# Performance work log

Measured on AMD Instinct MI355X. Metric: run time of the kernel, lower is better.

## Reference

```python
import jax, jax.numpy as jnp
import numpy as np

B, T, I, H = 1024, 64, 64, 1024
FUTURE = 16


def lstm_cell(x_t, h, c, Wih, Whh, b_ih, b_hh):
    # torch LSTMCell gate order: i, f, g, o; weights are (4H, in)
    gates = x_t @ Wih.T + h @ Whh.T + b_ih + b_hh  # (B, 4H)
    i, f, g, o = jnp.split(gates, 4, axis=-1)
    i = jax.nn.sigmoid(i)
    f = jax.nn.sigmoid(f)
    g = jnp.tanh(g)
    o = jax.nn.sigmoid(o)
    c_new = f * c + i * g
    h_new = o * jnp.tanh(c_new)
    return h_new, c_new


def setup_inputs() -> dict:
    key = jax.random.key(0)
    ks = jax.random.split(key, 12)
    s1 = 1.0 / np.sqrt(H)
    inp = {
        "x": jax.random.normal(ks[0], (B, T, I), dtype=jnp.float32),
        "W_ih1": jax.random.uniform(ks[1], (4 * H, I), jnp.float32, -s1, s1),
        "W_hh1": jax.random.uniform(ks[2], (4 * H, H), jnp.float32, -s1, s1),
        "b_ih1": jax.random.uniform(ks[3], (4 * H,), jnp.float32, -s1, s1),
        "b_hh1": jax.random.uniform(ks[4], (4 * H,), jnp.float32, -s1, s1),
        "W_ih2": jax.random.uniform(ks[5], (4 * H, H), jnp.float32, -s1, s1),
        "W_hh2": jax.random.uniform(ks[6], (4 * H, H), jnp.float32, -s1, s1),
        "b_ih2": jax.random.uniform(ks[7], (4 * H,), jnp.float32, -s1, s1),
        "b_hh2": jax.random.uniform(ks[8], (4 * H,), jnp.float32, -s1, s1),
        "W_lin": jax.random.uniform(ks[9], (I, H), jnp.float32, -s1, s1),
        "b_lin": jax.random.uniform(ks[10], (I,), jnp.float32, -s1, s1),
        "future": FUTURE,
    }
    return inp


def reference(x, W_ih1, W_hh1, b_ih1, b_hh1, W_ih2, W_hh2, b_ih2, b_hh2,
              W_lin, b_lin, future):
    b_size = x.shape[0]
    zeros = jnp.zeros((b_size, H), dtype=x.dtype)

    def two_layer_step(h1, c1, h2, c2, x_t):
        h1, c1 = lstm_cell(x_t, h1, c1, W_ih1, W_hh1, b_ih1, b_hh1)
        h2, c2 = lstm_cell(h1, h2, c2, W_ih2, W_hh2, b_ih2, b_hh2)
        out = h2 @ W_lin.T + b_lin  # (B, I)
        return h1, c1, h2, c2, out

    def step(carry, x_t):
        h1, c1, h2, c2 = carry
        h1, c1, h2, c2, out = two_layer_step(h1, c1, h2, c2, x_t)
        return (h1, c1, h2, c2), out

    xs = jnp.transpose(x, (1, 0, 2))  # (T, B, I)
    carry, outs = jax.lax.scan(step, (zeros, zeros, zeros, zeros), xs)

    if future > 0:
        def fstep(carry, _):
            h1, c1, h2, c2, out = carry
            h1, c1, h2, c2, out = two_layer_step(h1, c1, h2, c2, out)
            return (h1, c1, h2, c2, out), out

        h1, c1, h2, c2 = carry
        _, fouts = jax.lax.scan(fstep, (h1, c1, h2, c2, outs[-1]),
                                None, length=future)
        outs = jnp.concatenate([outs, fouts], axis=0)

    return jnp.transpose(outs, (1, 0, 2))  # (B, T+future, I)
```

## Files before the change

### kernel.cpp

```cpp
#include <hip/hip_runtime.h>


#define B_   1024
#define T_   64
#define I_   64
#define H_   1024
#define FUT_ 16
#define NST_ (T_ + FUT_)
#define SROW 2176

typedef _Float16 half8_t  __attribute__((ext_vector_type(8)));
typedef float    float4_t __attribute__((ext_vector_type(4)));

typedef __attribute__((address_space(1))) const unsigned int g_u32;
typedef __attribute__((address_space(3))) unsigned int l_u32;

__device__ __forceinline__ void load_lds16(const _Float16* g, _Float16* l) {
    __builtin_amdgcn_global_load_lds((g_u32*)g, (l_u32*)l, 16, 0, 0);
}

__device__ __forceinline__ float sigmoid_f(float x) {
    x = fminf(fmaxf(x, -30.f), 30.f);
    return __fdividef(1.f, 1.f + __expf(-x));
}
__device__ __forceinline__ float tanh_f(float x) {
    x = fminf(fmaxf(x, -15.f), 15.f);
    float e = __expf(2.f * x);
    return 1.f - 2.f * __fdividef(1.f, e + 1.f);
}

__global__ void convert_all(const float* __restrict__ x,
    const float* __restrict__ Wih1, const float* __restrict__ Whh1,
    const float* __restrict__ bih1, const float* __restrict__ bhh1,
    const float* __restrict__ Wih2, const float* __restrict__ Whh2,
    const float* __restrict__ bih2, const float* __restrict__ bhh2,
    const float* __restrict__ Wlin,
    _Float16* __restrict__ W1p, _Float16* __restrict__ W2p,
    _Float16* __restrict__ Wlp,
    _Float16* __restrict__ S0x, _Float16* __restrict__ S1x,
    float* __restrict__ b1, float* __restrict__ b2)
{
    size_t idx = (size_t)blockIdx.x * 256 + threadIdx.x;
    const size_t nc1 = 589824;
    const size_t nc2 = 1048576;
    const size_t nc3 = 8192;
    const size_t nx  = 65536;
    if (idx < nc1) {
        int c = (int)idx;
        int lane = c & 63, g = (c >> 6) & 3, rem = c >> 8;
        int j = rem % 36, hgrp = rem / 36;
        int row = (g << 10) + hgrp * 16 + (lane & 15);
        int kb = j * 32 + (lane >> 4) * 8;
        _Float16* o = &W1p[(size_t)c * 8];
        if (kb < 1024) {
            #pragma unroll
            for (int i = 0; i < 8; ++i) o[i] = (_Float16)Whh1[(size_t)row * 1024 + kb + i];
        } else if (kb < 1088) {
            #pragma unroll
            for (int i = 0; i < 8; ++i) o[i] = (_Float16)Wih1[row * 64 + (kb - 1024) + i];
        } else {
            #pragma unroll
            for (int i = 0; i < 8; ++i) o[i] = (_Float16)0.f;
        }
    } else if ((idx -= nc1) < nc2) {
        int c = (int)idx;
        int lane = c & 63, g = (c >> 6) & 3, rem = c >> 8;
        int j = rem & 63, hgrp = rem >> 6;
        int row = (g << 10) + hgrp * 16 + (lane & 15);
        int kb = j * 32 + (lane >> 4) * 8;
        _Float16* o = &W2p[(size_t)c * 8];
        if (kb < 1024) {
            #pragma unroll
            for (int i = 0; i < 8; ++i) o[i] = (_Float16)Wih2[(size_t)row * 1024 + kb + i];
        } else {
            #pragma unroll
            for (int i = 0; i < 8; ++i) o[i] = (_Float16)Whh2[(size_t)row * 1024 + kb - 1024 + i];
        }
    } else if ((idx -= nc2) < nc3) {
        int c = (int)idx;
        int lane = c & 63, j = (c >> 6) & 31, hgrp = c >> 11;
        int row = hgrp * 16 + (lane & 15);
        int kb = j * 32 + (lane >> 4) * 8;
        _Float16* o = &Wlp[(size_t)c * 8];
        #pragma unroll
        for (int i = 0; i < 8; ++i) o[i] = (_Float16)Wlin[(size_t)row * 1024 + kb + i];
    } else if ((idx -= nc3) < nx) {
        int b = (int)(idx >> 6), i = (int)(idx & 63);
        S0x[(size_t)b * SROW + i] = (_Float16)x[(size_t)b * (T_ * I_) + i];
    } else if ((idx -= nx) < nx) {
        int b = (int)(idx >> 6), i = (int)(idx & 63);
        S1x[(size_t)b * SROW + i] = (_Float16)x[(size_t)b * (T_ * I_) + 64 + i];
    } else if ((idx -= nx) < 4096) {
        b1[idx] = bih1[idx] + bhh1[idx];
    } else if ((idx -= 4096) < 4096) {
        b2[idx] = bih2[idx] + bhh2[idx];
    }
}

__device__ __forceinline__ void gemm_body(_Float16* sA,
    const _Float16* __restrict__ Alo, const _Float16* __restrict__ Ahi,
    const _Float16* __restrict__ Wp, const int iters, const int Ksh,
    const float* __restrict__ bias, float* __restrict__ cvec,
    _Float16* __restrict__ hdst, const int unit)
{
    const int tid = threadIdx.x;
    const int lane = tid & 63, w = tid >> 6;
    const int hw = w & 1, kh = w >> 1;
    const int lr = lane & 15, lq = lane >> 4;
    const int ht = ((unit & 7) << 2) | ((unit >> 3) & 3);
    const int mt = unit >> 5;
    const int h0 = ht * 32, m0 = mt * 64;
    const int hgrp = ht * 2 + hw;

    const char* wptr = (const char*)Wp
        + ((size_t)hgrp * (2 * Ksh) + (size_t)kh * Ksh) * 4096
        + (size_t)lane * 16;

    const int srow0 = tid >> 4, pg = tid & 15;
    const int gg = pg ^ (srow0 & 15);
    const _Float16* asrc = (gg < 8 ? Alo : Ahi) + (gg & 7) * 8
                         + (size_t)(m0 + srow0) * SROW;
    _Float16* ldst = sA + tid * 8;

    const int ag0 = ((kh * 8 + lq) ^ lr) * 8;
    const int ag1 = ((kh * 8 + 4 + lq) ^ lr) * 8;

    float4_t acc[4][4];
    #pragma unroll
    for (int g = 0; g < 4; ++g)
        #pragma unroll
        for (int rt = 0; rt < 4; ++rt)
            #pragma unroll
            for (int e = 0; e < 4; ++e) acc[g][rt][e] = 0.f;

    half8_t bfc[8], bfn[8];
    #pragma unroll
    for (int q = 0; q < 8; ++q)
        bfc[q] = *(const half8_t*)(wptr + q * 1024);

    for (int i = 0; i < iters; ++i) {
        #pragma unroll
        for (int s = 0; s < 4; ++s)
            load_lds16(asrc + (size_t)(srow0 + s * 16 - srow0) * 0
                       + (size_t)s * 16 * SROW + (size_t)i * 64,
                       ldst + s * 2048);
        __syncthreads();

        if (i + 1 < iters) {
            const char* wn = wptr + 8192;
            #pragma unroll
            for (int q = 0; q < 8; ++q)
                bfn[q] = *(const half8_t*)(wn + q * 1024);
        }
        #pragma unroll
        for (int ks = 0; ks < 2; ++ks) {
            const int ag = ks ? ag1 : ag0;
            half8_t af[4];
            #pragma unroll
            for (int rt = 0; rt < 4; ++rt)
                af[rt] = *(const half8_t*)&sA[(rt * 16 + lr) * 128 + ag];
            #pragma unroll
            for (int g = 0; g < 4; ++g)
                #pragma unroll
                for (int rt = 0; rt < 4; ++rt)
                    acc[g][rt] = __builtin_amdgcn_mfma_f32_16x16x32_f16(
                        af[rt], bfc[ks * 4 + g], acc[g][rt], 0, 0, 0);
        }
        __syncthreads();
        wptr += 8192;
        #pragma unroll
        for (int q = 0; q < 8; ++q) bfc[q] = bfn[q];
    }

    float* scr = (float*)sA;
    #pragma unroll
    for (int gp = 0; gp < 2; ++gp) {
        if (kh == 1) {
            #pragma unroll
            for (int g2 = 0; g2 < 2; ++g2)
                #pragma unroll
                for (int rt = 0; rt < 4; ++rt) {
                    int slot = ((hw * 2 + g2) * 4 + rt) * 64 + lane;
                    *(float4_t*)&scr[slot * 4] = acc[gp * 2 + g2][rt];
                }
        }
        __syncthreads();
        if (kh == 0) {
            #pragma unroll
            for (int g2 = 0; g2 < 2; ++g2)
                #pragma unroll
                for (int rt = 0; rt < 4; ++rt) {
                    int slot = ((hw * 2 + g2) * 4 + rt) * 64 + lane;
                    acc[gp * 2 + g2][rt] += *(const float4_t*)&scr[slot * 4];
                }
        }
        __syncthreads();
    }
    if (kh != 0) return;

    const int j = h0 + hw * 16 + lr;
    const float bi = bias[j], bff = bias[1024 + j];
    const float bg = bias[2048 + j], bo = bias[3072 + j];
    #pragma unroll
    for (int rt = 0; rt < 4; ++rt) {
        #pragma unroll
        for (int e = 0; e < 4; ++e) {
            const int brow = m0 + rt * 16 + lq * 4 + e;
            float gi = sigmoid_f(acc[0][rt][e] + bi);
            float gf = sigmoid_f(acc[1][rt][e] + bff);
            float gv = tanh_f(acc[2][rt][e] + bg);
            float go = sigmoid_f(acc[3][rt][e] + bo);
            const size_t ci = (size_t)brow * 1024 + j;
            float cn = gf * cvec[ci] + gi * gv;
            cvec[ci] = cn;
            hdst[(size_t)brow * SROW + j] = (_Float16)(go * tanh_f(cn));
        }
    }
}

__device__ __forceinline__ void proj_body(_Float16* sA,
    const _Float16* __restrict__ A, const _Float16* __restrict__ Wp,
    const float* __restrict__ blin, float* __restrict__ outp,
    _Float16* __restrict__ xdst, const int unit)
{
    const int iters = 8;
    const int tid = threadIdx.x;
    const int lane = tid & 63, w = tid >> 6;
    const int hw = w & 1, kh = w >> 1;
    const int lr = lane & 15, lq = lane >> 4;
    const int ht = unit & 1, mt = unit >> 1;
    const int h0 = ht * 32, m0 = mt * 64;
    const int hgrp = ht * 2 + hw;

    const char* wptr = (const char*)Wp
        + ((size_t)hgrp * 32 + (size_t)kh * 16) * 1024 + (size_t)lane * 16;

    const int srow0 = tid >> 4, pg = tid & 15;
    const int gg = pg ^ (srow0 & 15);
    const _Float16* asrc = A + (size_t)(gg >> 3) * 512 + (gg & 7) * 8
                         + (size_t)(m0 + srow0) * SROW;
    _Float16* ldst = sA + tid * 8;
    const int ag0 = ((kh * 8 + lq) ^ lr) * 8;
    const int ag1 = ((kh * 8 + 4 + lq) ^ lr) * 8;

    float4_t acc[4];
    #pragma unroll
    for (int rt = 0; rt < 4; ++rt)
        #pragma unroll
        for (int e = 0; e < 4; ++e) acc[rt][e] = 0.f;

    half8_t b0 = *(const half8_t*)(wptr);
    half8_t b1v = *(const half8_t*)(wptr + 1024);
    for (int i = 0; i < iters; ++i) {
        #pragma unroll
        for (int s = 0; s < 4; ++s)
            load_lds16(asrc + (size_t)s * 16 * SROW + (size_t)i * 64,
                       ldst + s * 2048);
        __syncthreads();
        half8_t n0, n1;
        if (i + 1 < iters) {
            n0 = *(const half8_t*)(wptr + 2048);
            n1 = *(const half8_t*)(wptr + 3072);
        }
        half8_t af;
        #pragma unroll
        for (int rt = 0; rt < 4; ++rt) {
            af = *(const half8_t*)&sA[(rt * 16 + lr) * 128 + ag0];
            acc[rt] = __builtin_amdgcn_mfma_f32_16x16x32_f16(af, b0, acc[rt], 0, 0, 0);
        }
        #pragma unroll
        for (int rt = 0; rt < 4; ++rt) {
            af = *(const half8_t*)&sA[(rt * 16 + lr) * 128 + ag1];
            acc[rt] = __builtin_amdgcn_mfma_f32_16x16x32_f16(af, b1v, acc[rt], 0, 0, 0);
        }
        __syncthreads();
        wptr += 2048;
        b0 = n0; b1v = n1;
    }

    float* scr = (float*)sA;
    if (kh == 1) {
        #pragma unroll
        for (int rt = 0; rt < 4; ++rt) {
            int slot = (hw * 4 + rt) * 64 + lane;
            *(float4_t*)&scr[slot * 4] = acc[rt];
        }
    }
    __syncthreads();
    if (kh != 0) return;
    #pragma unroll
    for (int rt = 0; rt < 4; ++rt) {
        int slot = (hw * 4 + rt) * 64 + lane;
        acc[rt] += *(const float4_t*)&scr[slot * 4];
    }

    const int j = h0 + hw * 16 + lr;
    const float bj = blin[j];
    #pragma unroll
    for (int rt = 0; rt < 4; ++rt) {
        #pragma unroll
        for (int e = 0; e < 4; ++e) {
            const int brow = m0 + rt * 16 + lq * 4 + e;
            float s = acc[rt][e] + bj;
            outp[(size_t)brow * (NST_ * I_) + j] = s;
            if (xdst) xdst[(size_t)brow * SROW + j] = (_Float16)s;
        }
    }
}

struct StepArgs {
    int nL2, nL1, nProj, nCopy;
    const _Float16 *l2Alo, *l2Ahi; _Float16* l2H; float* c2;
    const _Float16 *l1Alo, *l1Ahi; _Float16* l1H; float* c1;
    const _Float16* pA; float* pOut; _Float16* pXdst;
    const float* xsrc; _Float16* xdst;
    const _Float16 *W1p, *W2p, *Wlp;
    const float *b1, *b2, *blin;
};

__global__ __launch_bounds__(256, 3) void fused_step(StepArgs a) {
    __shared__ __align__(16) _Float16 sA[8192];
    int bid = blockIdx.x;
    if (bid < a.nL2) {
        gemm_body(sA, a.l2Alo, a.l2Ahi, a.W2p, 16, 32, a.b2, a.c2, a.l2H, bid);
    } else if ((bid -= a.nL2) < a.nL1) {
        gemm_body(sA, a.l1Alo, a.l1Ahi, a.W1p, 9, 18, a.b1, a.c1, a.l1H, bid);
    } else if ((bid -= a.nL1) < a.nProj) {
        proj_body(sA, a.pA, a.Wlp, a.blin, a.pOut, a.pXdst, bid);
    } else {
        bid -= a.nProj;
        int base = bid * 256 + threadIdx.x;
        for (int k = base; k < B_ * I_; k += a.nCopy * 256) {
            int b = k >> 6, i = k & 63;
            a.xdst[(size_t)b * SROW + i] = (_Float16)a.xsrc[(size_t)b * (T_ * I_) + i];
        }
    }
}

extern "C" void kernel_launch(void* const* d_in, const int* in_sizes, int n_in,
                              void* d_out, int out_size, void* d_ws, size_t ws_size,
                              hipStream_t stream) {
    (void)in_sizes; (void)n_in; (void)out_size; (void)ws_size;
    const float* x    = (const float*)d_in[0];
    const float* Wih1 = (const float*)d_in[1];
    const float* Whh1 = (const float*)d_in[2];
    const float* bih1 = (const float*)d_in[3];
    const float* bhh1 = (const float*)d_in[4];
    const float* Wih2 = (const float*)d_in[5];
    const float* Whh2 = (const float*)d_in[6];
    const float* bih2 = (const float*)d_in[7];
    const float* bhh2 = (const float*)d_in[8];
    const float* Wlin = (const float*)d_in[9];
    const float* blin = (const float*)d_in[10];
    float* out = (float*)d_out;

    char* p = (char*)d_ws;
    auto alloc = [&](size_t bytes) {
        char* r = p; p += (bytes + 255) & ~(size_t)255; return r;
    };
    _Float16* W1p = (_Float16*)alloc((size_t)4096 * 1152 * 2);
    _Float16* W2p = (_Float16*)alloc((size_t)4096 * 2048 * 2);
    _Float16* Wlp = (_Float16*)alloc((size_t)64 * 1024 * 2);
    _Float16* S[3];
    for (int i = 0; i < 3; ++i) S[i] = (_Float16*)alloc((size_t)B_ * SROW * 2);
    float* c1 = (float*)alloc((size_t)B_ * H_ * 4);
    float* c2 = (float*)alloc((size_t)B_ * H_ * 4);
    float* b1 = (float*)alloc(4096 * 4);
    float* b2 = (float*)alloc(4096 * 4);

    for (int i = 0; i < 3; ++i)
        hipMemsetAsync(S[i], 0, (size_t)B_ * SROW * 2, stream);
    hipMemsetAsync(c1, 0, (size_t)B_ * H_ * 4, stream);
    hipMemsetAsync(c2, 0, (size_t)B_ * H_ * 4, stream);

    {
        const size_t total = 589824 + 1048576 + 8192 + 65536 + 65536 + 8192;
        convert_all<<<(int)((total + 255) / 256), 256, 0, stream>>>(
            x, Wih1, Whh1, bih1, bhh1, Wih2, Whh2, bih2, bhh2, Wlin,
            W1p, W2p, Wlp, S[0] + 1024, S[1] + 1024, b1, b2);
    }

    StepArgs a{};
    a.W1p = W1p; a.W2p = W2p; a.Wlp = Wlp;
    a.b1 = b1; a.b2 = b2; a.blin = blin;
    a.c1 = c1; a.c2 = c2;

    {
        StepArgs q = a;
        q.nL2 = 0; q.nL1 = 512; q.nProj = 0; q.nCopy = 0;
        q.l1Alo = S[0]; q.l1Ahi = S[0] + 576; q.l1H = S[1];
        fused_step<<<512, 256, 0, stream>>>(q);
    }

    for (int t = 0; t <= 62; ++t) {
        _Float16* Sp = S[t % 3];
        _Float16* Sq = S[(t + 1) % 3];
        _Float16* Sn = S[(t + 2) % 3];
        StepArgs q = a;
        q.nL2 = 512; q.nL1 = 512;
        q.nProj = (t >= 1) ? 32 : 0;
        q.nCopy = (t <= 61) ? 16 : 0;
        q.l2Alo = Sq; q.l2Ahi = Sp + 1152; q.l2H = Sq + 1152;
        q.l1Alo = Sq; q.l1Ahi = Sq + 576; q.l1H = Sn;
        q.pA = Sp + 1152; q.pOut = out + (size_t)(t - 1) * I_; q.pXdst = nullptr;
        q.xsrc = x + (size_t)(t + 2) * I_; q.xdst = Sn + 1024;
        int grid = q.nL2 + q.nL1 + q.nProj + q.nCopy;
        fused_step<<<grid, 256, 0, stream>>>(q);
    }

    {
        StepArgs q = a;
        q.nL2 = 512; q.nL1 = 0; q.nProj = 32; q.nCopy = 0;
        q.l2Alo = S[1]; q.l2Ahi = S[0] + 1152; q.l2H = S[1] + 1152;
        q.pA = S[0] + 1152; q.pOut = out + (size_t)62 * I_; q.pXdst = nullptr;
        fused_step<<<544, 256, 0, stream>>>(q);
    }
    {
        StepArgs q = a;
        q.nL2 = 0; q.nL1 = 0; q.nProj = 32; q.nCopy = 0;
        q.pA = S[1] + 1152; q.pOut = out + (size_t)63 * I_; q.pXdst = S[1] + 1024;
        fused_step<<<32, 256, 0, stream>>>(q);
    }

    for (int t = T_; t < NST_; ++t) {
        _Float16* Sp = S[t % 3];
        _Float16* Sq = S[(t + 1) % 3];
        {
            StepArgs q = a;
            q.nL2 = 0; q.nL1 = 512; q.nProj = 0; q.nCopy = 0;
            q.l1Alo = Sp; q.l1Ahi = Sp + 576; q.l1H = Sq;
            fused_step<<<512, 256, 0, stream>>>(q);
        }
        {
            StepArgs q = a;
            q.nL2 = 512; q.nL1 = 0; q.nProj = 0; q.nCopy = 0;
            q.l2Alo = Sq; q.l2Ahi = Sp + 1152; q.l2H = Sq + 1152;
            fused_step<<<512, 256, 0, stream>>>(q);
        }
        {
            StepArgs q = a;
            q.nL2 = 0; q.nL1 = 0; q.nProj = 32; q.nCopy = 0;
            q.pA = Sq + 1152; q.pOut = out + (size_t)t * I_;
            q.pXdst = (t + 1 < NST_) ? (Sq + 1024) : nullptr;
            fused_step<<<32, 256, 0, stream>>>(q);
        }
    }
}
```

Before: 3.686 ms.

## Fold output projection into layer-1 weights for future steps and double-buffer LDS

For the autoregressive future steps, the layer-1 input weights are precomposed with the linear projection (W_ih1·W_lin, with bias folded in), so layer 1 reads h2 directly instead of waiting for a separate projection kernel. Each future step drops from three launches to two, and the projection output now runs alongside the layer-1 GEMM. Separately, the GEMM A-tile staging is double-buffered in LDS, removing one barrier per k-iteration, which doubles shared memory per block. The composed weights are rounded to fp16 after the product, which changes rounding relative to the reference path.

Result: faster. 3.561 ms (-3.4%).

```diff
diff --git a/kernel.cpp b/kernel.cpp
--- a/kernel.cpp
+++ b/kernel.cpp
@@ -97,7 +97,44 @@
     }
 }
 
-__device__ __forceinline__ void gemm_body(_Float16* sA,
+__global__ void compose_pack(const float* __restrict__ Wih1,
+    const float* __restrict__ Whh1, const float* __restrict__ Wlin,
+    const float* __restrict__ blin, const float* __restrict__ b1in,
+    _Float16* __restrict__ W1c2, float* __restrict__ bc1)
+{
+    size_t idx = (size_t)blockIdx.x * 256 + threadIdx.x;
+    const size_t NC = 1048576;
+    if (idx < NC) {
+        int c = (int)idx;
+        int lane = c & 63, g = (c >> 6) & 3, rem = c >> 8;
+        int j = rem & 63, hgrp = rem >> 6;
+        int row = (g << 10) + hgrp * 16 + (lane & 15);
+        int kb = j * 32 + (lane >> 4) * 8;
+        _Float16* o = &W1c2[(size_t)c * 8];
+        if (kb < 1024) {
+            #pragma unroll
+            for (int i = 0; i < 8; ++i) o[i] = (_Float16)Whh1[(size_t)row * 1024 + kb + i];
+        } else {
+            const int h = kb - 1024;
+            float acc[8] = {0, 0, 0, 0, 0, 0, 0, 0};
+            for (int i2 = 0; i2 < 64; ++i2) {
+                float wv = Wih1[row * 64 + i2];
+                const float* wl = &Wlin[(size_t)i2 * 1024 + h];
+                #pragma unroll
+                for (int e = 0; e < 8; ++e) acc[e] += wv * wl[e];
+            }
+            #pragma unroll
+            for (int e = 0; e < 8; ++e) o[e] = (_Float16)acc[e];
+        }
+    } else if ((idx -= NC) < 4096) {
+        int n = (int)idx;
+        float s = b1in[n];
+        for (int i2 = 0; i2 < 64; ++i2) s += Wih1[n * 64 + i2] * blin[i2];
+        bc1[n] = s;
+    }
+}
+
+__device__ __forceinline__ void gemm_body(_Float16* sAb,
     const _Float16* __restrict__ Alo, const _Float16* __restrict__ Ahi,
     const _Float16* __restrict__ Wp, const int iters, const int Ksh,
     const float* __restrict__ bias, float* __restrict__ cvec,
@@ -120,7 +157,6 @@
     const int gg = pg ^ (srow0 & 15);
     const _Float16* asrc = (gg < 8 ? Alo : Ahi) + (gg & 7) * 8
                          + (size_t)(m0 + srow0) * SROW;
-    _Float16* ldst = sA + tid * 8;
 
     const int ag0 = ((kh * 8 + lq) ^ lr) * 8;
     const int ag1 = ((kh * 8 + 4 + lq) ^ lr) * 8;
@@ -138,15 +174,19 @@
     for (int q = 0; q < 8; ++q)
         bfc[q] = *(const half8_t*)(wptr + q * 1024);
 
+    #pragma unroll
+    for (int s = 0; s < 4; ++s)
+        load_lds16(asrc + (size_t)s * 16 * SROW, sAb + tid * 8 + s * 2048);
+
     for (int i = 0; i < iters; ++i) {
-        #pragma unroll
-        for (int s = 0; s < 4; ++s)
-            load_lds16(asrc + (size_t)(srow0 + s * 16 - srow0) * 0
-                       + (size_t)s * 16 * SROW + (size_t)i * 64,
-                       ldst + s * 2048);
         __syncthreads();
-
+        _Float16* cur = sAb + (i & 1) * 8192;
         if (i + 1 < iters) {
+            _Float16* nxt = sAb + ((i + 1) & 1) * 8192;
+            const _Float16* an = asrc + (size_t)(i + 1) * 64;
+            #pragma unroll
+            for (int s = 0; s < 4; ++s)
+                load_lds16(an + (size_t)s * 16 * SROW, nxt + tid * 8 + s * 2048);
             const char* wn = wptr + 8192;
             #pragma unroll
             for (int q = 0; q < 8; ++q)
@@ -155,24 +195,22 @@
         #pragma unroll
         for (int ks = 0; ks < 2; ++ks) {
             const int ag = ks ? ag1 : ag0;
-            half8_t af[4];
-            #pragma unroll
-            for (int rt = 0; rt < 4; ++rt)
-                af[rt] = *(const half8_t*)&sA[(rt * 16 + lr) * 128 + ag];
-            #pragma unroll
-            for (int g = 0; g < 4; ++g)
+            #pragma unroll
+            for (int rt = 0; rt < 4; ++rt) {
+                half8_t af = *(const half8_t*)&cur[(rt * 16 + lr) * 128 + ag];
                 #pragma unroll
-                for (int rt = 0; rt < 4; ++rt)
+                for (int g = 0; g < 4; ++g)
                     acc[g][rt] = __builtin_amdgcn_mfma_f32_16x16x32_f16(
-                        af[rt], bfc[ks * 4 + g], acc[g][rt], 0, 0, 0);
-        }
-        __syncthreads();
+                        af, bfc[ks * 4 + g], acc[g][rt], 0, 0, 0);
+            }
+        }
         wptr += 8192;
         #pragma unroll
         for (int q = 0; q < 8; ++q) bfc[q] = bfn[q];
     }
-
-    float* scr = (float*)sA;
+    __syncthreads();
+
+    float* scr = (float*)sAb;
     #pragma unroll
     for (int gp = 0; gp < 2; ++gp) {
         if (kh == 1) {
@@ -221,7 +259,7 @@
 __device__ __forceinline__ void proj_body(_Float16* sA,
     const _Float16* __restrict__ A, const _Float16* __restrict__ Wp,
     const float* __restrict__ blin, float* __restrict__ outp,
-    _Float16* __restrict__ xdst, const int unit)
+    const int unit)
 {
     const int iters = 8;
     const int tid = threadIdx.x;
@@ -301,32 +339,32 @@
         #pragma unroll
         for (int e = 0; e < 4; ++e) {
             const int brow = m0 + rt * 16 + lq * 4 + e;
-            float s = acc[rt][e] + bj;
-            outp[(size_t)brow * (NST_ * I_) + j] = s;
-            if (xdst) xdst[(size_t)brow * SROW + j] = (_Float16)s;
+            outp[(size_t)brow * (NST_ * I_) + j] = acc[rt][e] + bj;
         }
     }
 }
 
 struct StepArgs {
     int nL2, nL1, nProj, nCopy;
-    const _Float16 *l2Alo, *l2Ahi; _Float16* l2H; float* c2;
-    const _Float16 *l1Alo, *l1Ahi; _Float16* l1H; float* c1;
-    const _Float16* pA; float* pOut; _Float16* pXdst;
+    const _Float16 *l2Alo, *l2Ahi; _Float16* l2H; const float* l2b; float* c2;
+    const _Float16 *l1Alo, *l1Ahi; _Float16* l1H; const float* l1b; float* c1;
+    int l1Iters, l1Ksh; const _Float16* l1W;
+    const _Float16* pA; float* pOut;
     const float* xsrc; _Float16* xdst;
-    const _Float16 *W1p, *W2p, *Wlp;
-    const float *b1, *b2, *blin;
+    const _Float16 *W2p, *Wlp;
+    const float* blin;
 };
 
 __global__ __launch_bounds__(256, 3) void fused_step(StepArgs a) {
-    __shared__ __align__(16) _Float16 sA[8192];
+    __shared__ __align__(16) _Float16 sA[16384];
     int bid = blockIdx.x;
     if (bid < a.nL2) {
-        gemm_body(sA, a.l2Alo, a.l2Ahi, a.W2p, 16, 32, a.b2, a.c2, a.l2H, bid);
+        gemm_body(sA, a.l2Alo, a.l2Ahi, a.W2p, 16, 32, a.l2b, a.c2, a.l2H, bid);
     } else if ((bid -= a.nL2) < a.nL1) {
-        gemm_body(sA, a.l1Alo, a.l1Ahi, a.W1p, 9, 18, a.b1, a.c1, a.l1H, bid);
+        gemm_body(sA, a.l1Alo, a.l1Ahi, a.l1W, a.l1Iters, a.l1Ksh,
+                  a.l1b, a.c1, a.l1H, bid);
     } else if ((bid -= a.nL1) < a.nProj) {
-        proj_body(sA, a.pA, a.Wlp, a.blin, a.pOut, a.pXdst, bid);
+        proj_body(sA, a.pA, a.Wlp, a.blin, a.pOut, bid);
     } else {
         bid -= a.nProj;
         int base = bid * 256 + threadIdx.x;
@@ -358,15 +396,17 @@
     auto alloc = [&](size_t bytes) {
         char* r = p; p += (bytes + 255) & ~(size_t)255; return r;
     };
-    _Float16* W1p = (_Float16*)alloc((size_t)4096 * 1152 * 2);
-    _Float16* W2p = (_Float16*)alloc((size_t)4096 * 2048 * 2);
-    _Float16* Wlp = (_Float16*)alloc((size_t)64 * 1024 * 2);
+    _Float16* W1p  = (_Float16*)alloc((size_t)4096 * 1152 * 2);
+    _Float16* W2p  = (_Float16*)alloc((size_t)4096 * 2048 * 2);
+    _Float16* W1c2 = (_Float16*)alloc((size_t)4096 * 2048 * 2);
+    _Float16* Wlp  = (_Float16*)alloc((size_t)64 * 1024 * 2);
     _Float16* S[3];
     for (int i = 0; i < 3; ++i) S[i] = (_Float16*)alloc((size_t)B_ * SROW * 2);
-    float* c1 = (float*)alloc((size_t)B_ * H_ * 4);
-    float* c2 = (float*)alloc((size_t)B_ * H_ * 4);
-    float* b1 = (float*)alloc(4096 * 4);
-    float* b2 = (float*)alloc(4096 * 4);
+    float* c1  = (float*)alloc((size_t)B_ * H_ * 4);
+    float* c2  = (float*)alloc((size_t)B_ * H_ * 4);
+    float* b1  = (float*)alloc(4096 * 4);
+    float* b2  = (float*)alloc(4096 * 4);
+    float* bc1 = (float*)alloc(4096 * 4);
 
     for (int i = 0; i < 3; ++i)
         hipMemsetAsync(S[i], 0, (size_t)B_ * SROW * 2, stream);
@@ -378,12 +418,14 @@
         convert_all<<<(int)((total + 255) / 256), 256, 0, stream>>>(
             x, Wih1, Whh1, bih1, bhh1, Wih2, Whh2, bih2, bhh2, Wlin,
             W1p, W2p, Wlp, S[0] + 1024, S[1] + 1024, b1, b2);
+        compose_pack<<<(int)((1048576 + 4096 + 255) / 256), 256, 0, stream>>>(
+            Wih1, Whh1, Wlin, blin, b1, W1c2, bc1);
     }
 
     StepArgs a{};
-    a.W1p = W1p; a.W2p = W2p; a.Wlp = Wlp;
-    a.b1 = b1; a.b2 = b2; a.blin = blin;
-    a.c1 = c1; a.c2 = c2;
+    a.W2p = W2p; a.Wlp = Wlp; a.blin = blin;
+    a.l2b = b2; a.c2 = c2; a.l1b = b1; a.c1 = c1;
+    a.l1W = W1p; a.l1Iters = 9; a.l1Ksh = 18;
 
     {
         StepArgs q = a;
@@ -402,7 +444,7 @@
         q.nCopy = (t <= 61) ? 16 : 0;
         q.l2Alo = Sq; q.l2Ahi = Sp + 1152; q.l2H = Sq + 1152;
         q.l1Alo = Sq; q.l1Ahi = Sq + 576; q.l1H = Sn;
-        q.pA = Sp + 1152; q.pOut = out + (size_t)(t - 1) * I_; q.pXdst = nullptr;
+        q.pA = Sp + 1152; q.pOut = out + (size_t)(t - 1) * I_;
         q.xsrc = x + (size_t)(t + 2) * I_; q.xdst = Sn + 1024;
         int grid = q.nL2 + q.nL1 + q.nProj + q.nCopy;
         fused_step<<<grid, 256, 0, stream>>>(q);
@@ -412,24 +454,20 @@
         StepArgs q = a;
         q.nL2 = 512; q.nL1 = 0; q.nProj = 32; q.nCopy = 0;
         q.l2Alo = S[1]; q.l2Ahi = S[0] + 1152; q.l2H = S[1] + 1152;
-        q.pA = S[0] + 1152; q.pOut = out + (size_t)62 * I_; q.pXdst = nullptr;
+        q.pA = S[0] + 1152; q.pOut = out + (size_t)62 * I_;
         fused_step<<<544, 256, 0, stream>>>(q);
     }
-    {
-        StepArgs q = a;
-        q.nL2 = 0; q.nL1 = 0; q.nProj = 32; q.nCopy = 0;
-        q.pA = S[1] + 1152; q.pOut = out + (size_t)63 * I_; q.pXdst = S[1] + 1024;
-        fused_step<<<32, 256, 0, stream>>>(q);
-    }
 
     for (int t = T_; t < NST_; ++t) {
-        _Float16* Sp = S[t % 3];
-        _Float16* Sq = S[(t + 1) % 3];
+        _Float16* Sp = S[1 + ((t - T_) & 1)];
+        _Float16* Sq = S[1 + (((t - T_) & 1) ^ 1)];
         {
             StepArgs q = a;
-            q.nL2 = 0; q.nL1 = 512; q.nProj = 0; q.nCopy = 0;
-            q.l1Alo = Sp; q.l1Ahi = Sp + 576; q.l1H = Sq;
-            fused_step<<<512, 256, 0, stream>>>(q);
+            q.nL2 = 0; q.nL1 = 512; q.nProj = 32; q.nCopy = 0;
+            q.l1W = W1c2; q.l1Iters = 16; q.l1Ksh = 32; q.l1b = bc1;
+            q.l1Alo = Sp; q.l1Ahi = Sp + 1152; q.l1H = Sq;
+            q.pA = Sp + 1152; q.pOut = out + (size_t)(t - 1) * I_;
+            fused_step<<<544, 256, 0, stream>>>(q);
         }
         {
             StepArgs q = a;
@@ -437,12 +475,13 @@
             q.l2Alo = Sq; q.l2Ahi = Sp + 1152; q.l2H = Sq + 1152;
             fused_step<<<512, 256, 0, stream>>>(q);
         }
-        {
-            StepArgs q = a;
-            q.nL2 = 0; q.nL1 = 0; q.nProj = 32; q.nCopy = 0;
-            q.pA = Sq + 1152; q.pOut = out + (size_t)t * I_;
-            q.pXdst = (t + 1 < NST_) ? (Sq + 1024) : nullptr;
-            fused_step<<<32, 256, 0, stream>>>(q);
-        }
-    }
-}
+    }
+
+    {
+        _Float16* Sl = S[1 + (((NST_ - 1 - T_) & 1) ^ 1)];
+        StepArgs q = a;
+        q.nL2 = 0; q.nL1 = 0; q.nProj = 32; q.nCopy = 0;
+        q.pA = Sl + 1152; q.pOut = out + (size_t)(NST_ - 1) * I_;
+        fused_step<<<32, 256, 0, stream>>>(q);
+    }
+}
```
